# Kernel tuning notes

Hardware: AMD Instinct MI355X
Metric: run time of the kernel (lower is better)

The kernel has to match this reference:

```python
import jax, jax.numpy as jnp
import numpy as np

B, FEW, NN = 4096, 5, 64
D = 128            # embed_dim
NSYM = 100000
DM = 2 * D         # d_model = 256
DI = 2 * DM        # support-encoder inner = 512
H = 2 * DM         # LSTMCell hidden = 512
STEPS = 4          # process_steps


def setup_inputs() -> dict:
    key = jax.random.key(0)
    cnt = [0]
    def nk():
        cnt[0] += 1
        return jax.random.fold_in(key, cnt[0])
    def nrm(shape, scale=0.05):
        return jax.random.normal(nk(), shape, dtype=jnp.float32) * scale
    def ridx(shape):
        return jax.random.randint(nk(), shape, 0, NSYM, dtype=jnp.int32)
    inp = {}
    inp['q_l1'] = ridx((B, NN, 2)); inp['q_l2'] = ridx((B, NN, 2))
    inp['q_r1'] = ridx((B, NN, 2)); inp['q_r2'] = ridx((B, NN, 2))
    inp['s_l1'] = ridx((FEW, NN, 2)); inp['s_l2'] = ridx((FEW, NN, 2))
    inp['s_r1'] = ridx((FEW, NN, 2)); inp['s_r2'] = ridx((FEW, NN, 2))
    inp['q_deg_l'] = jax.random.randint(nk(), (B,), 1, NN, dtype=jnp.int32)
    inp['q_deg_r'] = jax.random.randint(nk(), (B,), 1, NN, dtype=jnp.int32)
    inp['s_deg_l'] = jax.random.randint(nk(), (FEW,), 1, NN, dtype=jnp.int32)
    inp['s_deg_r'] = jax.random.randint(nk(), (FEW,), 1, NN, dtype=jnp.int32)
    inp['emb'] = nrm((NSYM + 1, D)).at[NSYM].set(0.0)  # padding_idx row = 0
    inp['gcn_w'] = nrm((D, 2 * D))
    inp['gcn_wb'] = nrm((D,))
    inp['gcn_b'] = jnp.zeros((D,), jnp.float32)
    inp['hop_gate'] = jnp.ones((2,), jnp.float32)
    inp['attn_w'] = nrm((1, D))
    inp['attn_b'] = jnp.zeros((1,), jnp.float32)
    inp['p1_w'] = nrm((DI, DM)); inp['p1_b'] = jnp.zeros((DI,), jnp.float32)
    inp['p2_w'] = nrm((DM, DI)); inp['p2_b'] = jnp.zeros((DM,), jnp.float32)
    inp['ln_g'] = jnp.ones((DM,), jnp.float32); inp['ln_b'] = jnp.zeros((DM,), jnp.float32)
    inp['w_ih'] = nrm((4 * H, DM)); inp['w_hh'] = nrm((4 * H, H))
    inp['b_ih'] = jnp.zeros((4 * H,), jnp.float32); inp['b_hh'] = jnp.zeros((4 * H,), jnp.float32)
    return inp


def _neighbor_encoder(conn, emb, gcn_w, gcn_wb, gcn_b, attn_w, attn_b):
    # conn: [N, NN, 2] (relation id, entity id)
    e = emb[conn]                                     # [N, NN, 2, D]
    concat = e.reshape(conn.shape[0], conn.shape[1], 2 * D)  # cat(rel, ent)
    proj = concat @ gcn_w.T + gcn_wb + gcn_b          # [N, NN, D]
    scores = (proj @ attn_w.T + attn_b)[..., 0]       # [N, NN]
    w = jax.nn.softmax(scores, axis=1)[..., None]
    return jnp.tanh(jnp.sum(proj * w, axis=1))        # [N, D]


def _support_encoder(x, p1_w, p1_b, p2_w, p2_b, ln_g, ln_b):
    out = jax.nn.relu(x @ p1_w.T + p1_b) @ p2_w.T + p2_b
    z = out + x
    mu = jnp.mean(z, axis=-1, keepdims=True)
    var = jnp.var(z, axis=-1, keepdims=True)
    return (z - mu) / jnp.sqrt(var + 1e-6) * ln_g + ln_b


def _query_encoder(support_g, q, w_ih, w_hh, b_ih, b_hh):
    # matching-networks 'process' LSTM attention, STEPS fixed iterations
    h_r = jnp.zeros((q.shape[0], H), q.dtype)
    c = jnp.zeros_like(h_r)
    h = q
    for _ in range(STEPS):
        gates = q @ w_ih.T + b_ih + h_r @ w_hh.T + b_hh
        i, f, g, o = jnp.split(gates, 4, axis=-1)
        c = jax.nn.sigmoid(f) * c + jax.nn.sigmoid(i) * jnp.tanh(g)
        h_cell = jax.nn.sigmoid(o) * jnp.tanh(c)
        h = q + h_cell[:, :DM]
        attn = jax.nn.softmax(h @ support_g.T, axis=1)
        r = attn @ support_g
        h_r = jnp.concatenate([h, r], axis=1)
    return h


def reference(q_l1, q_l2, q_r1, q_r2, s_l1, s_l2, s_r1, s_r2,
              q_deg_l, q_deg_r, s_deg_l, s_deg_r,
              emb, gcn_w, gcn_wb, gcn_b, hop_gate, attn_w, attn_b,
              p1_w, p1_b, p2_w, p2_b, ln_g, ln_b, w_ih, w_hh, b_ih, b_hh):
    ne = lambda conn: _neighbor_encoder(conn, emb, gcn_w, gcn_wb, gcn_b, attn_w, attn_b)
    gw = jax.nn.softmax(hop_gate)
    q_left = gw[0] * ne(q_l1) + gw[1] * ne(q_l2)
    q_right = gw[0] * ne(q_r1) + gw[1] * ne(q_r2)
    s_left = gw[0] * ne(s_l1) + gw[1] * ne(s_l2)
    s_right = gw[0] * ne(s_r1) + gw[1] * ne(s_r2)
    query_neighbor = jnp.concatenate([q_left, q_right], axis=-1)    # [B, DM]
    support_neighbor = jnp.concatenate([s_left, s_right], axis=-1)  # [FEW, DM]
    support_g = _support_encoder(support_neighbor, p1_w, p1_b, p2_w, p2_b, ln_g, ln_b)
    query_g = _query_encoder(support_g, query_neighbor, w_ih, w_hh, b_ih, b_hh)
    support_m = jnp.mean(support_g, axis=0, keepdims=True)          # [1, DM]
    return (query_g @ support_m.T)[:, 0]                            # [B]
```

## Files before the change

kernel.cpp:

```cpp
#include <hip/hip_runtime.h>

typedef unsigned short bf16u;
typedef unsigned char u8;
typedef unsigned int u32;
typedef float f32x4 __attribute__((ext_vector_type(4)));
typedef short bf16x8 __attribute__((ext_vector_type(8)));

__device__ inline float sigmoidf_(float x) { return 1.f / (1.f + __expf(-x)); }
__device__ inline float tanhf_(float x) {
  float e = __expf(2.f * x);
  return 1.f - 2.f / (e + 1.f);
}
__device__ inline float b2f(bf16u u) { return __uint_as_float(((u32)u) << 16); }
__device__ inline bf16u f2b(float f) {
  u32 i = __float_as_uint(f);
  u32 r = (i + 0x7fffu + ((i >> 16) & 1u)) >> 16;
  return (bf16u)r;
}
__device__ inline u8 enc8(float v) {
  float q = fmaf(v, 512.f, 128.5f);
  q = fminf(fmaxf(q, 0.f), 255.f);
  return (u8)(int)q;
}
__device__ inline float ub0(u32 u) { return (float)(u & 0xffu); }
__device__ inline float ub1(u32 u) { return (float)((u >> 8) & 0xffu); }
__device__ inline float ub2(u32 u) { return (float)((u >> 16) & 0xffu); }
__device__ inline float ub3(u32 u) { return (float)(u >> 24); }

__global__ __launch_bounds__(256) void k_prep(
    const float* __restrict__ gcn_w, const float* __restrict__ attn_w,
    const float* __restrict__ w_ih, const float* __restrict__ w_hh,
    const float* __restrict__ b_ih, const float* __restrict__ b_hh,
    bf16u* __restrict__ Vp, float* __restrict__ uvec,
    bf16u* __restrict__ WWa, bf16u* __restrict__ WWb, float* __restrict__ bsum,
    bf16u* __restrict__ XX)
{
  const int b = blockIdx.x, t = threadIdx.x;
  if (t < 59) XX[(size_t)b * 576 + 517 + t] = 0;
  if (b < 2048) {
    float wi = w_ih[b * 256 + t];
    float wh = w_hh[b * 512 + t];
    WWa[(size_t)b * 576 + t] = f2b(wi);
    WWb[(size_t)b * 576 + t] = f2b(wi + wh);
    WWb[(size_t)b * 576 + 256 + t] = f2b(wh);
    if (t < 59) WWb[(size_t)b * 576 + 517 + t] = 0;
    if (t == 0) bsum[b] = b_ih[b] + b_hh[b];
  } else if (b < 2304) {
    const int o = b - 2048;
    if (t < 128) Vp[o * 128 + t] = f2b(gcn_w[(o & 127) * 256 + ((o >> 7) << 7) + t]);
  } else if (b == 2304) {
    const int col = ((t >> 7) << 7) + (t & 127);
    float acc = 0.f;
    for (int d = 0; d < 128; ++d) acc += gcn_w[d * 256 + col] * attn_w[d];
    uvec[t] = acc;
  }
}

__global__ __launch_bounds__(256) void k_pre_gemm(
    const float* __restrict__ emb, const bf16u* __restrict__ Vp,
    const float* __restrict__ uvec,
    u8* __restrict__ pr, u8* __restrict__ pe,
    float* __restrict__ srel, float* __restrict__ sent)
{
  const int t = threadIdx.x;
  const int row0 = blockIdx.x << 6;
  __shared__ short As[64][136];
  __shared__ union PB {
    short B[128][136];
    u8 ob[64][272];
  } pb;
  __shared__ float us[256];
  us[t] = uvec[t];
  {
    const uint4* src = (const uint4*)Vp;
    #pragma unroll
    for (int s = 0; s < 8; ++s) {
      int f = s * 256 + t;
      *(uint4*)&pb.B[f >> 4][(f & 15) * 8] = src[f];
    }
  }
  #pragma unroll
  for (int s = 0; s < 8; ++s) {
    int f = s * 256 + t;
    int row = f >> 5, q = f & 31;
    int gr = row0 + row; if (gr > 100000) gr = 100000;
    float4 v = *(const float4*)&emb[(size_t)gr * 128 + (q << 2)];
    ushort4 pk;
    pk.x = f2b(v.x); pk.y = f2b(v.y); pk.z = f2b(v.z); pk.w = f2b(v.w);
    *(ushort4*)&As[row][q << 2] = pk;
  }
  __syncthreads();
  {
    const int row = t >> 2, l = t & 3;
    int gr = row0 + row; if (gr > 100000) gr = 100000;
    const short* ar = &As[row][l * 32];
    const float* u0 = &us[l * 32];
    const float* u1 = &us[128 + l * 32];
    float p0 = 0.f, p1 = 0.f;
    #pragma unroll
    for (int i = 0; i < 32; ++i) {
      float e = __uint_as_float(((u32)(unsigned short)ar[i]) << 16);
      p0 += e * u0[i];
      p1 += e * u1[i];
    }
    p0 += __shfl_xor(p0, 1, 64); p0 += __shfl_xor(p0, 2, 64);
    p1 += __shfl_xor(p1, 1, 64); p1 += __shfl_xor(p1, 2, 64);
    if (l == 0) { srel[gr] = p0; sent[gr] = p1; }
  }
  const int wave = t >> 6, lane = t & 63;
  const int quad = lane >> 4, l16 = lane & 15;
  const int wm = (wave >> 1) << 5, wn = (wave & 1) << 6;
  f32x4 acc0[2][4], acc1[2][4];
  #pragma unroll
  for (int i = 0; i < 2; ++i)
    #pragma unroll
    for (int j = 0; j < 4; ++j) {
      acc0[i][j] = (f32x4){0.f, 0.f, 0.f, 0.f};
      acc1[i][j] = (f32x4){0.f, 0.f, 0.f, 0.f};
    }
  #pragma unroll
  for (int kc = 0; kc < 4; ++kc) {
    bf16x8 af[2], bfr[4];
    #pragma unroll
    for (int i = 0; i < 2; ++i)
      af[i] = *(const bf16x8*)&As[wm + i * 16 + l16][kc * 32 + quad * 8];
    #pragma unroll
    for (int j = 0; j < 4; ++j)
      bfr[j] = *(const bf16x8*)&pb.B[wn + j * 16 + l16][kc * 32 + quad * 8];
    #pragma unroll
    for (int i = 0; i < 2; ++i)
      #pragma unroll
      for (int j = 0; j < 4; ++j)
        acc0[i][j] = __builtin_amdgcn_mfma_f32_16x16x32_bf16(af[i], bfr[j], acc0[i][j], 0, 0, 0);
  }
  __syncthreads();
  {
    const uint4* src = (const uint4*)(Vp + 128 * 128);
    #pragma unroll
    for (int s = 0; s < 8; ++s) {
      int f = s * 256 + t;
      *(uint4*)&pb.B[f >> 4][(f & 15) * 8] = src[f];
    }
  }
  __syncthreads();
  #pragma unroll
  for (int kc = 0; kc < 4; ++kc) {
    bf16x8 af[2], bfr[4];
    #pragma unroll
    for (int i = 0; i < 2; ++i)
      af[i] = *(const bf16x8*)&As[wm + i * 16 + l16][kc * 32 + quad * 8];
    #pragma unroll
    for (int j = 0; j < 4; ++j)
      bfr[j] = *(const bf16x8*)&pb.B[wn + j * 16 + l16][kc * 32 + quad * 8];
    #pragma unroll
    for (int i = 0; i < 2; ++i)
      #pragma unroll
      for (int j = 0; j < 4; ++j)
        acc1[i][j] = __builtin_amdgcn_mfma_f32_16x16x32_bf16(af[i], bfr[j], acc1[i][j], 0, 0, 0);
  }
  __syncthreads();
  #pragma unroll
  for (int j = 0; j < 4; ++j) {
    const int col = wn + j * 16 + l16;
    #pragma unroll
    for (int i = 0; i < 2; ++i) {
      #pragma unroll
      for (int r = 0; r < 4; ++r) {
        int row = wm + i * 16 + quad * 4 + r;
        pb.ob[row][col] = enc8(acc0[i][j][r]);
        pb.ob[row][128 + col] = enc8(acc1[i][j][r]);
      }
    }
  }
  __syncthreads();
  #pragma unroll
  for (int s = 0; s < 4; ++s) {
    int c = s * 256 + t;
    int row = c >> 4, part = c & 15;
    int gr = row0 + row;
    if (gr <= 100000) {
      uint4 v = *(const uint4*)&pb.ob[row][part * 16];
      if (part < 8) *(uint4*)&pr[(size_t)gr * 128 + part * 16] = v;
      else          *(uint4*)&pe[(size_t)gr * 128 + (part - 8) * 16] = v;
    }
  }
}

__global__ __launch_bounds__(256) void k_neighbor(
    const int* __restrict__ q_l1, const int* __restrict__ q_l2,
    const int* __restrict__ q_r1, const int* __restrict__ q_r2,
    const int* __restrict__ s_l1, const int* __restrict__ s_l2,
    const int* __restrict__ s_r1, const int* __restrict__ s_r2,
    const u8* __restrict__ pr, const u8* __restrict__ pe,
    const float* __restrict__ srel, const float* __restrict__ sent,
    const float* __restrict__ gcn_wb, const float* __restrict__ gcn_b,
    const float* __restrict__ hop_gate,
    float* __restrict__ qn, float* __restrict__ sn, bf16u* __restrict__ XX)
{
  const int b = blockIdx.x, t = threadIdx.x;
  const int *cA, *cB; float* outp; bf16u* xxp; int n, coloff;
  if (b < 4096)      { cA = q_l1; cB = q_l2; n = b;        outp = qn; xxp = XX; coloff = 0; }
  else if (b < 8192) { cA = q_r1; cB = q_r2; n = b - 4096; outp = qn; xxp = XX; coloff = 128; }
  else if (b < 8197) { cA = s_l1; cB = s_l2; n = b - 8192; outp = sn; xxp = 0;  coloff = 0; }
  else               { cA = s_r1; cB = s_r2; n = b - 8197; outp = sn; xxp = 0;  coloff = 128; }

  __shared__ float wS[2][64];
  __shared__ float red[256][17];

  const int hop = t >> 7, g = (t >> 3) & 15, p = t & 7;
  const int* connG = hop ? cB : cA;

  int2 pairs[4];
  #pragma unroll
  for (int kk = 0; kk < 4; ++kk)
    pairs[kk] = *(const int2*)&connG[(n * 64 + g + (kk << 4)) * 2];

  float vR = 0.f, vE = 0.f;
  if (t < 128) {
    const int sh = t >> 6, nn = t & 63;
    const int* connS = sh ? cB : cA;
    int2 sp = *(const int2*)&connS[(n * 64 + nn) * 2];
    vR = srel[sp.x];
    vE = sent[sp.y];
  }

  uint4 ra[4], rb[4];
  #pragma unroll
  for (int kk = 0; kk < 4; ++kk) {
    ra[kk] = *(const uint4*)&pr[(size_t)pairs[kk].x * 128 + p * 16];
    rb[kk] = *(const uint4*)&pe[(size_t)pairs[kk].y * 128 + p * 16];
  }

  if (t < 128) {
    const int sh = t >> 6, nn = t & 63;
    float sc = vR + vE;
    float m = sc;
    #pragma unroll
    for (int off = 32; off; off >>= 1) m = fmaxf(m, __shfl_xor(m, off, 64));
    float e = __expf(sc - m);
    float s = e;
    #pragma unroll
    for (int off = 32; off; off >>= 1) s += __shfl_xor(s, off, 64);
    wS[sh][nn] = e / s;
  }
  __syncthreads();

  float a[16];
  #pragma unroll
  for (int c = 0; c < 16; ++c) a[c] = 0.f;
  #pragma unroll
  for (int kk = 0; kk < 4; ++kk) {
    const float wk = wS[hop][g + (kk << 4)];
    const uint4 A = ra[kk], Bv = rb[kk];
    a[0]  += wk * (ub0(A.x) + ub0(Bv.x));
    a[1]  += wk * (ub1(A.x) + ub1(Bv.x));
    a[2]  += wk * (ub2(A.x) + ub2(Bv.x));
    a[3]  += wk * (ub3(A.x) + ub3(Bv.x));
    a[4]  += wk * (ub0(A.y) + ub0(Bv.y));
    a[5]  += wk * (ub1(A.y) + ub1(Bv.y));
    a[6]  += wk * (ub2(A.y) + ub2(Bv.y));
    a[7]  += wk * (ub3(A.y) + ub3(Bv.y));
    a[8]  += wk * (ub0(A.z) + ub0(Bv.z));
    a[9]  += wk * (ub1(A.z) + ub1(Bv.z));
    a[10] += wk * (ub2(A.z) + ub2(Bv.z));
    a[11] += wk * (ub3(A.z) + ub3(Bv.z));
    a[12] += wk * (ub0(A.w) + ub0(Bv.w));
    a[13] += wk * (ub1(A.w) + ub1(Bv.w));
    a[14] += wk * (ub2(A.w) + ub2(Bv.w));
    a[15] += wk * (ub3(A.w) + ub3(Bv.w));
  }
  #pragma unroll
  for (int c = 0; c < 16; ++c) red[t][c] = a[c];
  __syncthreads();

  if (t < 128) {
    const int d = t, pp = d >> 4, cc = d & 15;
    float sA = 0.f, sB = 0.f;
    #pragma unroll
    for (int gg = 0; gg < 16; ++gg) {
      sA += red[gg * 8 + pp][cc];
      sB += red[128 + gg * 8 + pp][cc];
    }
    float accA = sA * (1.f / 512.f) - 0.5f;
    float accB = sB * (1.f / 512.f) - 0.5f;
    float bias = gcn_wb[d] + gcn_b[d];
    float g0 = hop_gate[0], g1 = hop_gate[1];
    float mx = fmaxf(g0, g1);
    float e0 = __expf(g0 - mx), e1 = __expf(g1 - mx);
    float inv = 1.f / (e0 + e1);
    float v = e0 * inv * tanhf_(bias + accA) + e1 * inv * tanhf_(bias + accB);
    outp[n * 256 + coloff + d] = v;
    if (xxp) xxp[(size_t)n * 576 + coloff + d] = f2b(v);
  }
}

__global__ __launch_bounds__(256) void k_sup1(
    const float* __restrict__ sn, const float* __restrict__ p1_w,
    const float* __restrict__ p1_b, float* __restrict__ h1)
{
  const int r = blockIdx.x >> 3, j0 = (blockIdx.x & 7) << 6;
  const int t = threadIdx.x;
  __shared__ float xs[256];
  xs[t] = sn[r * 256 + t];
  __syncthreads();
  const int j = j0 + (t >> 2), q = t & 3;
  const float* wr = p1_w + (size_t)j * 256 + q * 64;
  float acc = 0.f;
  #pragma unroll
  for (int k = 0; k < 64; ++k) acc += xs[q * 64 + k] * wr[k];
  acc += __shfl_xor(acc, 1, 64);
  acc += __shfl_xor(acc, 2, 64);
  if (q == 0) h1[r * 512 + j] = fmaxf(acc + p1_b[j], 0.f);
}

__global__ __launch_bounds__(256) void k_sup2(
    const float* __restrict__ sn, const float* __restrict__ h1,
    const float* __restrict__ p2_w, const float* __restrict__ p2_b,
    const float* __restrict__ ln_g, const float* __restrict__ ln_b,
    float* __restrict__ sg)
{
  const int r = blockIdx.x, t = threadIdx.x;
  const int lane = t & 63, wave = t >> 6;
  __shared__ float hs[512];
  __shared__ float zs[256];
  __shared__ float r1[4], r2[4];
  hs[t] = h1[r * 512 + t];
  hs[t + 256] = h1[r * 512 + 256 + t];
  __syncthreads();
  const int q = t & 3;
  #pragma unroll
  for (int jc = 0; jc < 4; ++jc) {
    int j = jc * 64 + (t >> 2);
    const float* wr = p2_w + (size_t)j * 512 + q * 128;
    float acc = 0.f;
    #pragma unroll
    for (int k = 0; k < 128; ++k) acc += hs[q * 128 + k] * wr[k];
    acc += __shfl_xor(acc, 1, 64);
    acc += __shfl_xor(acc, 2, 64);
    if (q == 0) zs[j] = acc + p2_b[j] + sn[r * 256 + j];
  }
  __syncthreads();
  float v = zs[t];
  float s1 = v, s2 = v * v;
  #pragma unroll
  for (int off = 32; off; off >>= 1) { s1 += __shfl_xor(s1, off, 64); s2 += __shfl_xor(s2, off, 64); }
  if (lane == 0) { r1[wave] = s1; r2[wave] = s2; }
  __syncthreads();
  float S1 = r1[0] + r1[1] + r1[2] + r1[3];
  float S2 = r2[0] + r2[1] + r2[2] + r2[3];
  float mu = S1 * (1.f / 256.f);
  float var = S2 * (1.f / 256.f) - mu * mu;
  sg[r * 256 + t] = (v - mu) * rsqrtf(var + 1e-6f) * ln_g[t] + ln_b[t];
}

__global__ __launch_bounds__(256) void k_sg2(
    const float* __restrict__ sg, const float* __restrict__ w_hh,
    bf16u* __restrict__ WWb, float* __restrict__ sm)
{
  __shared__ float s[5][256];
  const int t = threadIdx.x;
  for (int i = t; i < 1280; i += 256) s[i >> 8][i & 255] = sg[i];
  __syncthreads();
  if (blockIdx.x == 0)
    sm[t] = (s[0][t] + s[1][t] + s[2][t] + s[3][t] + s[4][t]) * 0.2f;
  const int j = (blockIdx.x << 6) + (t >> 2), q = t & 3;
  const float4* wr = (const float4*)(w_hh + (size_t)j * 512 + 256 + q * 64);
  float a[5] = {0.f, 0.f, 0.f, 0.f, 0.f};
  #pragma unroll
  for (int kk = 0; kk < 16; ++kk) {
    float4 w = wr[kk];
    int k = q * 64 + kk * 4;
    #pragma unroll
    for (int r = 0; r < 5; ++r)
      a[r] += s[r][k] * w.x + s[r][k+1] * w.y + s[r][k+2] * w.z + s[r][k+3] * w.w;
  }
  #pragma unroll
  for (int r = 0; r < 5; ++r) {
    a[r] += __shfl_xor(a[r], 1, 64);
    a[r] += __shfl_xor(a[r], 2, 64);
  }
  if (q == 0) {
    #pragma unroll
    for (int r = 0; r < 5; ++r)
      WWb[(size_t)j * 576 + 512 + r] = f2b(a[r]);
  }
}

__global__ __launch_bounds__(256) void k_gates_mfma(
    const bf16u* __restrict__ XX, const bf16u* __restrict__ WW,
    const float* __restrict__ bsum, bf16u* __restrict__ gates, int kchunks)
{
  const int t = threadIdx.x;
  const int wave = t >> 6, lane = t & 63;
  const int quad = lane >> 4, l16 = lane & 15;
  const int wm = (wave >> 1) << 6, wn = (wave & 1) << 6;
  const int lin = (blockIdx.x & 7) * 56 + (blockIdx.x >> 3);
  const int row0 = (lin / 14) << 7;
  const int col0 = (lin % 14) << 7;
  __shared__ short As[2][128][40];
  __shared__ short Bs[2][128][40];
  f32x4 acc[4][4];
  #pragma unroll
  for (int i = 0; i < 4; ++i)
    #pragma unroll
    for (int j = 0; j < 4; ++j) acc[i][j] = (f32x4){0.f, 0.f, 0.f, 0.f};

  const int srow = t >> 1, shalf = t & 1;
  const bf16u* xp = XX + (size_t)(row0 + srow) * 576 + shalf * 16;
  const bf16u* wp = WW + (size_t)(col0 + srow) * 576 + shalf * 16;

  {
    uint4 x0 = *(const uint4*)(xp);
    uint4 x1 = *(const uint4*)(xp + 8);
    uint4 w0 = *(const uint4*)(wp);
    uint4 w1 = *(const uint4*)(wp + 8);
    *(uint4*)&As[0][srow][shalf * 16] = x0;
    *(uint4*)&As[0][srow][shalf * 16 + 8] = x1;
    *(uint4*)&Bs[0][srow][shalf * 16] = w0;
    *(uint4*)&Bs[0][srow][shalf * 16 + 8] = w1;
  }
  uint4 x0, x1, w0, w1;
  if (kchunks > 1) {
    x0 = *(const uint4*)(xp + 32);
    x1 = *(const uint4*)(xp + 40);
    w0 = *(const uint4*)(wp + 32);
    w1 = *(const uint4*)(wp + 40);
  }
  __syncthreads();

  for (int kc = 0; kc < kchunks; ++kc) {
    const int cur = kc & 1, nxt = cur ^ 1;
    if (kc + 1 < kchunks) {
      *(uint4*)&As[nxt][srow][shalf * 16] = x0;
      *(uint4*)&As[nxt][srow][shalf * 16 + 8] = x1;
      *(uint4*)&Bs[nxt][srow][shalf * 16] = w0;
      *(uint4*)&Bs[nxt][srow][shalf * 16 + 8] = w1;
    }
    if (kc + 2 < kchunks) {
      x0 = *(const uint4*)(xp + (kc+2) * 32);
      x1 = *(const uint4*)(xp + (kc+2) * 32 + 8);
      w0 = *(const uint4*)(wp + (kc+2) * 32);
      w1 = *(const uint4*)(wp + (kc+2) * 32 + 8);
    }
    bf16x8 af[4], bfr[4];
    #pragma unroll
    for (int i = 0; i < 4; ++i)
      af[i] = *(const bf16x8*)&As[cur][wm + i * 16 + l16][quad * 8];
    #pragma unroll
    for (int j = 0; j < 4; ++j)
      bfr[j] = *(const bf16x8*)&Bs[cur][wn + j * 16 + l16][quad * 8];
    #pragma unroll
    for (int i = 0; i < 4; ++i)
      #pragma unroll
      for (int j = 0; j < 4; ++j)
        acc[i][j] = __builtin_amdgcn_mfma_f32_16x16x32_bf16(af[i], bfr[j], acc[i][j], 0, 0, 0);
    __syncthreads();
  }

  #pragma unroll
  for (int j = 0; j < 4; ++j) {
    const int col = col0 + wn + j * 16 + l16;
    const float bs = bsum[col];
    #pragma unroll
    for (int i = 0; i < 4; ++i) {
      #pragma unroll
      for (int r = 0; r < 4; ++r) {
        int row = row0 + wm + i * 16 + quad * 4 + r;
        gates[(size_t)row * 2048 + col] = f2b(acc[i][j][r] + bs);
      }
    }
  }
}

__global__ __launch_bounds__(256) void k_cell(
    const bf16u* __restrict__ gates, const float* __restrict__ qn,
    float* __restrict__ c, bf16u* __restrict__ XX,
    const float* __restrict__ sg, const float* __restrict__ sm,
    float* __restrict__ out, int step)
{
  __shared__ float red[4][6];
  const int b = blockIdx.x, t = threadIdx.x;
  const int lane = t & 63, wave = t >> 6;
  const bf16u* g = gates + (size_t)b * 2048;
  float i0 = b2f(g[t]),       f0 = b2f(g[512 + t]), gg0 = b2f(g[1024 + t]), o0 = b2f(g[1536 + t]);
  float i1 = b2f(g[256 + t]), f1 = b2f(g[768 + t]), gg1 = b2f(g[1280 + t]);
  float co0 = step ? c[b * 512 + t] : 0.f;
  float co1 = step ? c[b * 512 + 256 + t] : 0.f;
  float c0 = sigmoidf_(f0) * co0 + sigmoidf_(i0) * tanhf_(gg0);
  float c1 = sigmoidf_(f1) * co1 + sigmoidf_(i1) * tanhf_(gg1);
  if (step < 3) {
    c[b * 512 + t] = c0;
    c[b * 512 + 256 + t] = c1;
  }
  float hcv = sigmoidf_(o0) * tanhf_(c0);
  float h = qn[b * 256 + t] + hcv;
  if (step < 3) {
    XX[(size_t)b * 576 + 256 + t] = f2b(hcv);
    float dots[5];
    #pragma unroll
    for (int s = 0; s < 5; ++s) dots[s] = h * sg[s * 256 + t];
    #pragma unroll
    for (int off = 32; off; off >>= 1) {
      #pragma unroll
      for (int s = 0; s < 5; ++s) dots[s] += __shfl_xor(dots[s], off, 64);
    }
    if (lane == 0) {
      #pragma unroll
      for (int s = 0; s < 5; ++s) red[wave][s] = dots[s];
    }
    __syncthreads();
    #pragma unroll
    for (int s = 0; s < 5; ++s)
      dots[s] = red[0][s] + red[1][s] + red[2][s] + red[3][s];
    float m = dots[0];
    #pragma unroll
    for (int s = 1; s < 5; ++s) m = fmaxf(m, dots[s]);
    float sum = 0.f;
    #pragma unroll
    for (int s = 0; s < 5; ++s) sum += __expf(dots[s] - m);
    if (t < 5) {
      float dv = (t == 1) ? dots[1] : (t == 2) ? dots[2] : (t == 3) ? dots[3]
               : (t == 4) ? dots[4] : dots[0];
      XX[(size_t)b * 576 + 512 + t] = f2b(__expf(dv - m) / sum);
    }
  } else {
    float v = h * sm[t];
    #pragma unroll
    for (int off = 32; off; off >>= 1) v += __shfl_xor(v, off, 64);
    if (lane == 0) red[wave][0] = v;
    __syncthreads();
    if (t == 0) out[b] = red[0][0] + red[1][0] + red[2][0] + red[3][0];
  }
}

extern "C" void kernel_launch(void* const* d_in, const int* in_sizes, int n_in,
                              void* d_out, int out_size, void* d_ws, size_t ws_size,
                              hipStream_t stream)
{
  (void)in_sizes; (void)n_in; (void)out_size; (void)ws_size;
  const int *q_l1 = (const int*)d_in[0], *q_l2 = (const int*)d_in[1];
  const int *q_r1 = (const int*)d_in[2], *q_r2 = (const int*)d_in[3];
  const int *s_l1 = (const int*)d_in[4], *s_l2 = (const int*)d_in[5];
  const int *s_r1 = (const int*)d_in[6], *s_r2 = (const int*)d_in[7];
  const float* emb      = (const float*)d_in[12];
  const float* gcn_w    = (const float*)d_in[13];
  const float* gcn_wb   = (const float*)d_in[14];
  const float* gcn_b    = (const float*)d_in[15];
  const float* hop_gate = (const float*)d_in[16];
  const float* attn_w   = (const float*)d_in[17];
  const float* p1_w = (const float*)d_in[19];
  const float* p1_b = (const float*)d_in[20];
  const float* p2_w = (const float*)d_in[21];
  const float* p2_b = (const float*)d_in[22];
  const float* ln_g = (const float*)d_in[23];
  const float* ln_b = (const float*)d_in[24];
  const float* w_ih = (const float*)d_in[25];
  const float* w_hh = (const float*)d_in[26];
  const float* b_ih = (const float*)d_in[27];
  const float* b_hh = (const float*)d_in[28];

  char* base = (char*)d_ws;
  size_t off = 0;
  auto alloc = [&](size_t bytes) -> char* {
    char* r = base + off;
    off = (off + bytes + 255) & ~(size_t)255;
    return r;
  };
  u8* pr       = (u8*)alloc(100001ull * 128);
  u8* pe       = (u8*)alloc(100001ull * 128);
  float* srel  = (float*)alloc(100001ull * 4);
  float* sent  = (float*)alloc(100001ull * 4);
  float* uvec  = (float*)alloc(256 * 4);
  bf16u* Vp    = (bf16u*)alloc(256 * 128 * 2);
  float* qn    = (float*)alloc(4096ull * 256 * 4);
  float* sn    = (float*)alloc(5 * 256 * 4);
  float* sg    = (float*)alloc(5 * 256 * 4);
  float* sm    = (float*)alloc(256 * 4);
  float* h1b   = (float*)alloc(5 * 512 * 4);
  bf16u* XX    = (bf16u*)alloc(4096ull * 576 * 2);
  bf16u* WWa   = (bf16u*)alloc(2048ull * 576 * 2);
  bf16u* WWb   = (bf16u*)alloc(2048ull * 576 * 2);
  float* bsum  = (float*)alloc(2048 * 4);
  bf16u* gates = (bf16u*)alloc(4096ull * 2048 * 2);
  float* cbuf  = (float*)alloc(4096ull * 512 * 4);

  k_prep<<<4096, 256, 0, stream>>>(gcn_w, attn_w, w_ih, w_hh, b_ih, b_hh,
                                   Vp, uvec, WWa, WWb, bsum, XX);
  k_pre_gemm<<<1563, 256, 0, stream>>>(emb, Vp, uvec, pr, pe, srel, sent);
  k_neighbor<<<8202, 256, 0, stream>>>(q_l1, q_l2, q_r1, q_r2, s_l1, s_l2, s_r1, s_r2,
                                       pr, pe, srel, sent, gcn_wb, gcn_b, hop_gate,
                                       qn, sn, XX);
  k_sup1<<<40, 256, 0, stream>>>(sn, p1_w, p1_b, h1b);
  k_sup2<<<5, 256, 0, stream>>>(sn, h1b, p2_w, p2_b, ln_g, ln_b, sg);
  k_sg2<<<32, 256, 0, stream>>>(sg, w_hh, WWb, sm);

  for (int step = 0; step < 4; ++step) {
    if (step == 0)
      k_gates_mfma<<<448, 256, 0, stream>>>(XX, WWa, bsum, gates, 8);
    else
      k_gates_mfma<<<448, 256, 0, stream>>>(XX, WWb, bsum, gates, 17);
    k_cell<<<4096, 256, 0, stream>>>(gates, qn, cbuf, XX, sg, sm, (float*)d_out, step);
  }
}
```

Measured before the change: 331.0 us.

## Use direct global-to-LDS loads with XOR-swizzled tiles in gates GEMM

Replaces the register-staged global loads and LDS stores in the gates MFMA GEMM with global_load_lds 16-byte direct transfers into shared memory. The padding of the LDS tiles is dropped and an XOR swizzle on the k-segment avoids bank conflicts instead. This is meant to cut VGPR use and instruction overhead for staging. The prefetch now sits one chunk ahead instead of two, and the async loads rely on __syncthreads to drain before use.

```diff
diff --git a/kernel.cpp b/kernel.cpp
--- a/kernel.cpp
+++ b/kernel.cpp
@@ -26,6 +26,11 @@
 __device__ inline float ub1(u32 u) { return (float)((u >> 8) & 0xffu); }
 __device__ inline float ub2(u32 u) { return (float)((u >> 16) & 0xffu); }
 __device__ inline float ub3(u32 u) { return (float)(u >> 24); }
+
+#define GLOAD16(gsrc, ldst)                                                   \
+  __builtin_amdgcn_global_load_lds(                                           \
+      (const __attribute__((address_space(1))) void*)(gsrc),                  \
+      (__attribute__((address_space(3))) void*)(ldst), 16, 0, 0)
 
 __global__ __launch_bounds__(256) void k_prep(
     const float* __restrict__ gcn_w, const float* __restrict__ attn_w,
@@ -397,58 +402,50 @@
   const int lin = (blockIdx.x & 7) * 56 + (blockIdx.x >> 3);
   const int row0 = (lin / 14) << 7;
   const int col0 = (lin % 14) << 7;
-  __shared__ short As[2][128][40];
-  __shared__ short Bs[2][128][40];
+  __shared__ short As[2][128][32];
+  __shared__ short Bs[2][128][32];
   f32x4 acc[4][4];
   #pragma unroll
   for (int i = 0; i < 4; ++i)
     #pragma unroll
     for (int j = 0; j < 4; ++j) acc[i][j] = (f32x4){0.f, 0.f, 0.f, 0.f};
 
-  const int srow = t >> 1, shalf = t & 1;
-  const bf16u* xp = XX + (size_t)(row0 + srow) * 576 + shalf * 16;
-  const bf16u* wp = WW + (size_t)(col0 + srow) * 576 + shalf * 16;
-
-  {
-    uint4 x0 = *(const uint4*)(xp);
-    uint4 x1 = *(const uint4*)(xp + 8);
-    uint4 w0 = *(const uint4*)(wp);
-    uint4 w1 = *(const uint4*)(wp + 8);
-    *(uint4*)&As[0][srow][shalf * 16] = x0;
-    *(uint4*)&As[0][srow][shalf * 16 + 8] = x1;
-    *(uint4*)&Bs[0][srow][shalf * 16] = w0;
-    *(uint4*)&Bs[0][srow][shalf * 16 + 8] = w1;
-  }
-  uint4 x0, x1, w0, w1;
-  if (kchunks > 1) {
-    x0 = *(const uint4*)(xp + 32);
-    x1 = *(const uint4*)(xp + 40);
-    w0 = *(const uint4*)(wp + 32);
-    w1 = *(const uint4*)(wp + 40);
-  }
-  __syncthreads();
-
+  int offX[2], offW[2];
+  #pragma unroll
+  for (int e = 0; e < 2; ++e) {
+    int s = wave * 128 + e * 64 + lane;
+    int row = s >> 2, qs = s & 3;
+    int sw = qs ^ ((row >> 1) & 3);
+    offX[e] = (row0 + row) * 576 + sw * 8;
+    offW[e] = (col0 + row) * 576 + sw * 8;
+  }
+  char* aBase = (char*)&As[0][0][0] + wave * 2048;
+  char* bBase = (char*)&Bs[0][0][0] + wave * 2048;
+
+  #define STAGE(buf, kc)                                                      \
+    {                                                                         \
+      const int kof_ = (kc) * 32;                                             \
+      _Pragma("unroll")                                                       \
+      for (int e = 0; e < 2; ++e) {                                           \
+        GLOAD16(XX + offX[e] + kof_, aBase + (buf) * 8192 + e * 1024);        \
+        GLOAD16(WW + offW[e] + kof_, bBase + (buf) * 8192 + e * 1024);        \
+      }                                                                       \
+    }
+
+  STAGE(0, 0);
+  __syncthreads();
+
+  const int swq = (quad ^ ((l16 >> 1) & 3)) << 3;
   for (int kc = 0; kc < kchunks; ++kc) {
-    const int cur = kc & 1, nxt = cur ^ 1;
-    if (kc + 1 < kchunks) {
-      *(uint4*)&As[nxt][srow][shalf * 16] = x0;
-      *(uint4*)&As[nxt][srow][shalf * 16 + 8] = x1;
-      *(uint4*)&Bs[nxt][srow][shalf * 16] = w0;
-      *(uint4*)&Bs[nxt][srow][shalf * 16 + 8] = w1;
-    }
-    if (kc + 2 < kchunks) {
-      x0 = *(const uint4*)(xp + (kc+2) * 32);
-      x1 = *(const uint4*)(xp + (kc+2) * 32 + 8);
-      w0 = *(const uint4*)(wp + (kc+2) * 32);
-      w1 = *(const uint4*)(wp + (kc+2) * 32 + 8);
-    }
+    const int cur = kc & 1;
+    if (kc + 1 < kchunks) STAGE(cur ^ 1, kc + 1);
     bf16x8 af[4], bfr[4];
     #pragma unroll
     for (int i = 0; i < 4; ++i)
-      af[i] = *(const bf16x8*)&As[cur][wm + i * 16 + l16][quad * 8];
+      af[i] = *(const bf16x8*)&As[cur][wm + i * 16 + l16][swq];
     #pragma unroll
     for (int j = 0; j < 4; ++j)
-      bfr[j] = *(const bf16x8*)&Bs[cur][wn + j * 16 + l16][quad * 8];
+      bfr[j] = *(const bf16x8*)&Bs[cur][wn + j * 16 + l16][swq];
     #pragma unroll
     for (int i = 0; i < 4; ++i)
       #pragma unroll
@@ -456,6 +453,7 @@
         acc[i][j] = __builtin_amdgcn_mfma_f32_16x16x32_bf16(af[i], bfr[j], acc[i][j], 0, 0, 0);
     __syncthreads();
   }
+  #undef STAGE
 
   #pragma unroll
   for (int j = 0; j < 4; ++j) {
```

New measurement: 334.8 us. About the same (+1.2%).
